# Kernel tuning notes

Measured on AMD Instinct MI355X. Metric: run time of the kernel, lower is better.

## Reference

```python
import jax, jax.numpy as jnp
import numpy as np

B, S, H = 16, 2048, 1024
N_EXAMPLES, MEM_LEN = 16, 128


def setup_inputs() -> dict:
    key = jax.random.key(0)
    k1, k2, k3, k4 = jax.random.split(key, 4)
    return {
        "seq_vectors": jax.random.normal(k1, (B, S, H), dtype=jnp.float32),
        "attention_mask": jax.random.randint(k2, (B, S), 0, 2, dtype=jnp.int32),
        "memory_vectors": jax.random.normal(k3, (B, N_EXAMPLES, MEM_LEN, H), dtype=jnp.float32),
        "memory_attention_mask": jax.random.randint(k4, (B, N_EXAMPLES, MEM_LEN), 0, 2, dtype=jnp.int32),
    }


def reference(seq_vectors, attention_mask, memory_vectors, memory_attention_mask):
    b, s, h = seq_vectors.shape
    # flatten memory: [B, N, H] with N = n_examples * mem_len
    mem = memory_vectors.reshape(b, -1, h)
    mmask = memory_attention_mask.reshape(b, -1)
    # zero out masked memory rows (mask-via-zero, not additive -inf)
    mem = jnp.where((mmask == 0)[:, :, None], jnp.zeros((), mem.dtype), mem)
    # FAITHFUL to original: view(batch, hidden, -1) is a RESHAPE of the
    # contiguous [B, N, H] buffer into [B, H, N], NOT a transpose.
    mem_reshaped = mem.reshape(b, h, -1)  # [B, H, N]
    scores = jnp.einsum("bsh,bhn->bsn", seq_vectors, mem_reshaped)  # [B, S, N]
    probs = jax.nn.softmax(scores, axis=-1)
    attention_vectors = jnp.einsum("bsn,bnh->bsh", probs, mem)
    return seq_vectors + attention_vectors
```

## Files before the change

kernel.cpp:

```cpp
#include <hip/hip_runtime.h>
#include <cstdint>
#include <cstddef>

#define Bn 16
#define Sn 2048
#define Hn 1024
#define Nn 2048

typedef unsigned short u16;
typedef float  f32x4  __attribute__((ext_vector_type(4)));
typedef int    i32x4  __attribute__((ext_vector_type(4)));
typedef short  s16x8  __attribute__((ext_vector_type(8)));
typedef unsigned char  u8x4  __attribute__((ext_vector_type(4)));
typedef unsigned char  u8x8  __attribute__((ext_vector_type(8)));

__device__ __forceinline__ void quant2(float x, char& q1, char& q2) {
  float f1 = rintf(x * 16.f);
  f1 = fminf(127.f, fmaxf(-127.f, f1));
  float r = x - f1 * 0.0625f;
  float f2 = rintf(r * 2048.f);
  f2 = fminf(127.f, fmaxf(-127.f, f2));
  q1 = (char)(int)f1;
  q2 = (char)(int)f2;
}

__device__ __forceinline__ char quant1(float x) {
  float f = rintf(x * 16.f);
  f = fminf(127.f, fmaxf(-127.f, f));
  return (char)(int)f;
}

__device__ __forceinline__ void stage64Bb(const char* gbase, int pitchBytes, void* ldsbase, int lane) {
  const int gsrc = (lane & 3) ^ ((lane >> 3) & 3);
  const char* gp = gbase + (size_t)(lane >> 2) * pitchBytes + gsrc * 16;
  __builtin_amdgcn_global_load_lds(
      (__attribute__((address_space(1))) void*)gp,
      (__attribute__((address_space(3))) void*)ldsbase, 16, 0, 0);
}


__global__ __launch_bounds__(256) void prep_seq_i8(const float* __restrict__ seq,
                                                   char* __restrict__ a1, char* __restrict__ a2) {
  size_t i = (size_t)blockIdx.x * 256 + threadIdx.x;
  float4 v = ((const float4*)seq)[i];
  float x[4] = {v.x, v.y, v.z, v.w};
  u8x4 p1, p2;
#pragma unroll
  for (int j = 0; j < 4; ++j) {
    char q1, q2;
    quant2(x[j], q1, q2);
    p1[j] = (unsigned char)q1;
    p2[j] = (unsigned char)q2;
  }
  ((u8x4*)a1)[i] = p1;
  ((u8x4*)a2)[i] = p2;
}

__global__ __launch_bounds__(256) void prep_bt(const float* __restrict__ mem,
                                               const int* __restrict__ mmask,
                                               char* __restrict__ b1o, char* __restrict__ b2o,
                                               char* __restrict__ memq) {
  __shared__ float tile[64][33];
  const int b = blockIdx.z;
  const int r0 = blockIdx.x * 64;
  const int c0 = blockIdx.y * 32;
  const int tx = threadIdx.x & 31, ty = threadIdx.x >> 5;
  const float* src = mem + (size_t)b * (Nn * Hn);
  const int* mk = mmask + b * Nn;
#pragma unroll
  for (int j = 0; j < 8; ++j) {
    int r = r0 + ty + j * 8;
    float v = src[(size_t)r * Hn + c0 + tx];
    v = mk[r] ? v : 0.f;
    tile[ty + j * 8][tx] = v;
  }
  __syncthreads();
  {
    const int nr = threadIdx.x >> 2;
    const int hb = (threadIdx.x & 3) * 8;
    u8x8 ov;
#pragma unroll
    for (int j = 0; j < 8; ++j) ov[j] = (unsigned char)quant1(tile[nr][hb + j]);
    *(u8x8*)(memq + (size_t)b * Nn * Hn + (size_t)(r0 + nr) * Hn + c0 + hb) = ov;
  }
  {
    const int cl = threadIdx.x & 31;
    const int p  = (threadIdx.x >> 5) & 1;
    const int q  = threadIdx.x >> 6;
    u8x8 o1, o2;
#pragma unroll
    for (int j = 0; j < 8; ++j) {
      char q1, q2;
      quant2(tile[2 * (q * 8 + j) + p][cl], q1, q2);
      o1[j] = (unsigned char)q1;
      o2[j] = (unsigned char)q2;
    }
    size_t o = (size_t)b * Nn * Hn + (size_t)(p * 1024 + c0 + cl) * Hn + (r0 >> 1) + q * 8;
    *(u8x8*)(b1o + o) = o1;
    *(u8x8*)(b2o + o) = o2;
  }
}

__global__ __launch_bounds__(256, 3) void gemm_scores_coarse(
    const char* __restrict__ A1, const char* __restrict__ B1,
    short* __restrict__ C) {
  __shared__ __align__(16) char ldsm[49152];
  const int b = blockIdx.z;
  const int lid = blockIdx.x + (blockIdx.y << 4);
  const int xcd = lid & 7, idx = lid >> 3;
  const int tn = ((xcd & 1) << 3) | (idx & 7);
  const int tm = ((xcd >> 1) << 2) | (idx >> 3);
  const int tid = threadIdx.x;
  const int w = tid >> 6, l = tid & 63;
  const int wr = w >> 1, wc = w & 1;
  const size_t aOff = (size_t)(b * Sn + tm * 128) * Hn;
  const size_t bOff = (size_t)(b * Nn + tn * 128) * Hn;

  i32x4 acc[4][4] = {};

  const int gRd = ((l >> 4) ^ ((l >> 1) & 3)) * 16;
  const int ao = (wr * 64 + (l & 15)) * 64 + gRd;
  const int bo = (wc * 64 + (l & 15)) * 64 + gRd;

  auto stageStep = [&](int kk, char* buf) {
    const int kb = kk * 64;
#pragma unroll
    for (int i = 0; i < 2; ++i) {
      const int rb = w * 32 + i * 16;
      const size_t ro = (size_t)rb * Hn + kb;
      stage64Bb(A1 + aOff + ro, Hn, buf + rb * 64, l);
      stage64Bb(B1 + bOff + ro, Hn, buf + 8192 + rb * 64, l);
    }
  };

  stageStep(0, ldsm);
  stageStep(1, ldsm + 16384);

  int cb = 0;
  for (int kk = 0; kk < 16; ++kk) {
    char* cur = ldsm + cb * 16384;
    int sb = cb + 2; if (sb >= 3) sb -= 3;
    if (kk <= 14) asm volatile("s_waitcnt vmcnt(4)" ::: "memory");
    else          asm volatile("s_waitcnt vmcnt(0)" ::: "memory");
    __builtin_amdgcn_s_barrier();
    asm volatile("" ::: "memory");
    __builtin_amdgcn_sched_barrier(0);
    i32x4 bfr[4];
#pragma unroll
    for (int ni = 0; ni < 4; ++ni) bfr[ni] = *(const i32x4*)(cur + 8192 + bo + ni * 1024);
    i32x4 afr[4];
#pragma unroll
    for (int mi = 0; mi < 4; ++mi) afr[mi] = *(const i32x4*)(cur + ao + mi * 1024);
    if (kk + 2 < 16) stageStep(kk + 2, ldsm + sb * 16384);
    __builtin_amdgcn_s_setprio(1);
#pragma unroll
    for (int mi = 0; mi < 4; ++mi)
#pragma unroll
      for (int ni = 0; ni < 4; ++ni)
        acc[mi][ni] = __builtin_amdgcn_mfma_i32_16x16x64_i8(afr[mi], bfr[ni], acc[mi][ni], 0, 0, 0);
    __builtin_amdgcn_s_setprio(0);
    cb = (cb + 1 == 3) ? 0 : cb + 1;
  }
  const int r0 = tm * 128 + wr * 64 + (l >> 4) * 4;
  const int c0 = tn * 128 + wc * 64 + (l & 15);
#pragma unroll
  for (int mi = 0; mi < 4; ++mi)
#pragma unroll
    for (int ni = 0; ni < 4; ++ni) {
      size_t base = (size_t)(b * Sn + r0 + mi * 16) * Nn + c0 + ni * 16;
#pragma unroll
      for (int j = 0; j < 4; ++j) {
        int s = (int)rintf((float)acc[mi][ni][j] * 0.5f);
        s = s > 32767 ? 32767 : (s < -32767 ? -32767 : s);
        C[base + (size_t)j * Nn] = (short)s;
      }
    }
}

__global__ __launch_bounds__(256) void softmax_attn(
    const short* __restrict__ sc,
    const char* __restrict__ memq,
    const char* __restrict__ B1q, const char* __restrict__ B2q,
    const char* __restrict__ A1q, const char* __restrict__ A2q,
    float* __restrict__ out) {
  __shared__ int redi[4];
  __shared__ int wtot[4];
  __shared__ unsigned short sidx[64];
  __shared__ int scand[64];
  __shared__ int scross[64];
  __shared__ unsigned char sp[64];
  const size_t row = blockIdx.x;
  const int b = (int)(row >> 11);
  const int t = threadIdx.x;
  const int w = t >> 6, l = t & 63;
  s16x8 v = ((const s16x8*)(sc + row * Nn))[t];
  int mymax = (int)v[0];
#pragma unroll
  for (int j = 1; j < 8; ++j) mymax = max(mymax, (int)v[j]);
  for (int o = 32; o > 0; o >>= 1) mymax = max(mymax, __shfl_xor(mymax, o));
  if (l == 0) redi[w] = mymax;
  __syncthreads();
  const int mc = max(max(redi[0], redi[1]), max(redi[2], redi[3]));
  const int thresh = mc - 1408;
  int cnt = 0;
#pragma unroll
  for (int j = 0; j < 8; ++j) cnt += ((int)v[j] >= thresh);
  int incl = cnt;
  for (int o = 1; o < 64; o <<= 1) {
    int xv = __shfl_up(incl, o);
    if (l >= o) incl += xv;
  }
  if (l == 63) wtot[w] = incl;
  __syncthreads();
  int base = 0;
#pragma unroll
  for (int wq = 0; wq < 4; ++wq) if (wq < w) base += wtot[wq];
  int pos = base + incl - cnt;
#pragma unroll
  for (int j = 0; j < 8; ++j)
    if ((int)v[j] >= thresh) {
      if (pos < 64) { sidx[pos] = (unsigned short)(t * 8 + j); scand[pos] = (int)v[j]; }
      pos++;
    }
  __syncthreads();
  int total = wtot[0] + wtot[1] + wtot[2] + wtot[3];
  if (total > 64) total = 64;
  const i32x4 a1s = *(const i32x4*)(A1q + row * (size_t)Hn + l * 16);
  const i32x4 a2s = *(const i32x4*)(A2q + row * (size_t)Hn + l * 16);
  for (int k0 = 0; k0 < total; k0 += 4) {
    const int k = k0 + w;
    int cross = 0;
    if (k < total) {
      const size_t nb = ((size_t)b * Nn + sidx[k]) * Hn + l * 16;
      const i32x4 b1v = *(const i32x4*)(B1q + nb);
      const i32x4 b2v = *(const i32x4*)(B2q + nb);
#pragma unroll
      for (int r = 0; r < 4; ++r)
#pragma unroll
        for (int s8 = 0; s8 < 4; ++s8) {
          const int sh = s8 * 8;
          cross += (int)(char)(a1s[r] >> sh) * (int)(char)(b2v[r] >> sh)
                 + (int)(char)(a2s[r] >> sh) * (int)(char)(b1v[r] >> sh);
        }
    }
    for (int o = 32; o > 0; o >>= 1) cross += __shfl_xor(cross, o);
    if (l == 0 && k < total) scross[k] = cross;
  }
  __syncthreads();
  if (t < total) {
    float mref = -1e30f;
    for (int k = 0; k < total; ++k) {
      float f = (float)scand[k] * 0.0078125f + (float)scross[k] * (1.f / 32768.f);
      mref = fmaxf(mref, f);
    }
    float s = 0.f;
    for (int k = 0; k < total; ++k) {
      float f = (float)scand[k] * 0.0078125f + (float)scross[k] * (1.f / 32768.f);
      s += __expf(f - mref);
    }
    const float fme = (float)scand[t] * 0.0078125f + (float)scross[t] * (1.f / 32768.f);
    sp[t] = (unsigned char)(int)rintf(127.f * __expf(fme - mref) / s);
  }
  __syncthreads();
  const char* mq = memq + (size_t)b * (Nn * Hn);
  int a0 = 0, a1v = 0, a2v = 0, a3 = 0;
  for (int k = 0; k < total; ++k) {
    const int pw = sp[k];
    if (!pw) continue;
    const int n = sidx[k];
    const int wv = *(const int*)(mq + (size_t)n * Hn + (t << 2));
    a0 += pw * (int)(char)(wv);
    a1v += pw * (int)(char)(wv >> 8);
    a2v += pw * (int)(char)(wv >> 16);
    a3 += pw * (int)(char)(wv >> 24);
  }
  const size_t obase = row * Hn + (size_t)(t << 2);
  const int w1 = *(const int*)(A1q + obase);
  const int w2 = *(const int*)(A2q + obase);
  const float scl = 1.f / 2032.f;
  float4 o;
  o.x = (float)(char)(w1)       * 0.0625f + (float)(char)(w2)       * (1.f / 2048.f) + (float)a0 * scl;
  o.y = (float)(char)(w1 >> 8)  * 0.0625f + (float)(char)(w2 >> 8)  * (1.f / 2048.f) + (float)a1v * scl;
  o.z = (float)(char)(w1 >> 16) * 0.0625f + (float)(char)(w2 >> 16) * (1.f / 2048.f) + (float)a2v * scl;
  o.w = (float)(char)(w1 >> 24) * 0.0625f + (float)(char)(w2 >> 24) * (1.f / 2048.f) + (float)a3 * scl;
  *(float4*)(out + obase) = o;
}

__global__ void ws_fail(float* out) {
  size_t i = (size_t)blockIdx.x * blockDim.x + threadIdx.x;
  size_t stride = (size_t)gridDim.x * blockDim.x;
  for (; i < (size_t)Bn * Sn * Hn; i += stride) out[i] = 12345.0f;
}

extern "C" void kernel_launch(void* const* d_in, const int* in_sizes, int n_in,
                              void* d_out, int out_size, void* d_ws, size_t ws_size,
                              hipStream_t stream) {
  const float* seq = (const float*)d_in[0];
  const float* mem = (const float*)d_in[2];
  const int* mmask = (const int*)d_in[3];
  float* out = (float*)d_out;

  const size_t MiB = 1024 * 1024;
  const size_t perB = 18 * MiB;
  int BC = 16;
  while (BC > 1 && (size_t)BC * perB > ws_size) BC >>= 1;
  if ((size_t)BC * perB > ws_size) {
    ws_fail<<<2048, 256, 0, stream>>>(out);
    return;
  }

  char* ws = (char*)d_ws;
  const size_t SEG8 = (size_t)BC * Sn * Hn;
  char* a1 = ws;
  char* a2 = ws + SEG8;
  char* b1 = ws + 2 * SEG8;
  char* b2 = ws + 3 * SEG8;
  char* memq = ws + 4 * SEG8;
  short* scores = (short*)(ws + 5 * SEG8);

  for (int b0 = 0; b0 < Bn; b0 += BC) {
    const float* seqb = seq + (size_t)b0 * Sn * Hn;
    const float* memb = mem + (size_t)b0 * Nn * Hn;
    const int* mkb = mmask + (size_t)b0 * Nn;
    float* outb = out + (size_t)b0 * Sn * Hn;

    prep_seq_i8<<<dim3(BC * Sn * Hn / 4 / 256), 256, 0, stream>>>(seqb, a1, a2);
    prep_bt<<<dim3(Nn / 64, Hn / 32, BC), 256, 0, stream>>>(memb, mkb, b1, b2, memq);
    gemm_scores_coarse<<<dim3(Nn / 128, Sn / 128, BC), 256, 0, stream>>>(a1, b1, scores);
    softmax_attn<<<dim3(BC * Sn), 256, 0, stream>>>(scores, memq, b1, b2, a1, a2, outb);
  }
}
```

Baseline: 362.8 us.

## Emit per-tile row maxima from scores GEMM to skip reading full score rows

The scores GEMM epilogue now reduces each row's maximum across its 128-column tile and writes it to a small per-row/per-tile buffer. The softmax kernel reads these 16 tile maxima to get the row max, then only loads the score tiles whose maximum reaches the threshold, instead of reading the whole 2048-wide score row. This is meant to cut score-buffer reads in the softmax stage. In exchange it adds shuffle and LDS reduction work to the GEMM epilogue and a serialized per-tile loop with three barriers per tile in softmax.

```diff
diff --git a/kernel.cpp b/kernel.cpp
--- a/kernel.cpp
+++ b/kernel.cpp
@@ -103,8 +103,9 @@
 
 __global__ __launch_bounds__(256, 3) void gemm_scores_coarse(
     const char* __restrict__ A1, const char* __restrict__ B1,
-    short* __restrict__ C) {
+    short* __restrict__ C, short* __restrict__ gtmax) {
   __shared__ __align__(16) char ldsm[49152];
+  __shared__ short tmx[2][128];
   const int b = blockIdx.z;
   const int lid = blockIdx.x + (blockIdx.y << 4);
   const int xcd = lid & 7, idx = lid >> 3;
@@ -175,16 +176,50 @@
         C[base + (size_t)j * Nn] = (short)s;
       }
     }
+  int rmax[4][4];
+#pragma unroll
+  for (int mi = 0; mi < 4; ++mi)
+#pragma unroll
+    for (int j = 0; j < 4; ++j) {
+      int mv = acc[mi][0][j];
+#pragma unroll
+      for (int ni = 1; ni < 4; ++ni) mv = max(mv, acc[mi][ni][j]);
+      rmax[mi][j] = mv;
+    }
+#pragma unroll
+  for (int o = 1; o < 16; o <<= 1)
+#pragma unroll
+    for (int mi = 0; mi < 4; ++mi)
+#pragma unroll
+      for (int j = 0; j < 4; ++j)
+        rmax[mi][j] = max(rmax[mi][j], __shfl_xor(rmax[mi][j], o));
+  if ((l & 15) == 0) {
+#pragma unroll
+    for (int mi = 0; mi < 4; ++mi)
+#pragma unroll
+      for (int j = 0; j < 4; ++j) {
+        int s = (int)rintf((float)rmax[mi][j] * 0.5f);
+        s = s > 32767 ? 32767 : (s < -32767 ? -32767 : s);
+        tmx[wc][wr * 64 + mi * 16 + (l >> 4) * 4 + j] = (short)s;
+      }
+  }
+  __syncthreads();
+  if (tid < 128) {
+    short mA = tmx[0][tid], mB = tmx[1][tid];
+    gtmax[(size_t)(b * Sn + tm * 128 + tid) * 16 + tn] = mA > mB ? mA : mB;
+  }
 }
 
 __global__ __launch_bounds__(256) void softmax_attn(
     const short* __restrict__ sc,
+    const short* __restrict__ tmax,
     const char* __restrict__ memq,
     const char* __restrict__ B1q, const char* __restrict__ B2q,
     const char* __restrict__ A1q, const char* __restrict__ A2q,
     float* __restrict__ out) {
-  __shared__ int redi[4];
+  __shared__ short sh16[16];
   __shared__ int wtot[4];
+  __shared__ int ncand_s;
   __shared__ unsigned short sidx[64];
   __shared__ int scand[64];
   __shared__ int scross[64];
@@ -193,38 +228,41 @@
   const int b = (int)(row >> 11);
   const int t = threadIdx.x;
   const int w = t >> 6, l = t & 63;
-  s16x8 v = ((const s16x8*)(sc + row * Nn))[t];
-  int mymax = (int)v[0];
-#pragma unroll
-  for (int j = 1; j < 8; ++j) mymax = max(mymax, (int)v[j]);
-  for (int o = 32; o > 0; o >>= 1) mymax = max(mymax, __shfl_xor(mymax, o));
-  if (l == 0) redi[w] = mymax;
-  __syncthreads();
-  const int mc = max(max(redi[0], redi[1]), max(redi[2], redi[3]));
+  if (t < 16) sh16[t] = tmax[row * 16 + t];
+  if (t == 0) ncand_s = 0;
+  __syncthreads();
+  int mc = -32768;
+#pragma unroll
+  for (int i = 0; i < 16; ++i) mc = max(mc, (int)sh16[i]);
   const int thresh = mc - 1408;
-  int cnt = 0;
-#pragma unroll
-  for (int j = 0; j < 8; ++j) cnt += ((int)v[j] >= thresh);
-  int incl = cnt;
-  for (int o = 1; o < 64; o <<= 1) {
-    int xv = __shfl_up(incl, o);
-    if (l >= o) incl += xv;
-  }
-  if (l == 63) wtot[w] = incl;
-  __syncthreads();
-  int base = 0;
-#pragma unroll
-  for (int wq = 0; wq < 4; ++wq) if (wq < w) base += wtot[wq];
-  int pos = base + incl - cnt;
-#pragma unroll
-  for (int j = 0; j < 8; ++j)
-    if ((int)v[j] >= thresh) {
-      if (pos < 64) { sidx[pos] = (unsigned short)(t * 8 + j); scand[pos] = (int)v[j]; }
-      pos++;
-    }
-  __syncthreads();
-  int total = wtot[0] + wtot[1] + wtot[2] + wtot[3];
-  if (total > 64) total = 64;
+  for (int ti = 0; ti < 16; ++ti) {
+    if ((int)sh16[ti] < thresh) continue;
+    int sval = 0, flag = 0;
+    if (t < 128) {
+      sval = (int)sc[row * (size_t)Nn + ti * 128 + t];
+      flag = (sval >= thresh) ? 1 : 0;
+    }
+    int incl = flag;
+    for (int o = 1; o < 64; o <<= 1) {
+      int xv = __shfl_up(incl, o);
+      if (l >= o) incl += xv;
+    }
+    if (l == 63) wtot[w] = incl;
+    __syncthreads();
+    const int base2 = ncand_s;
+    int basew = 0;
+#pragma unroll
+    for (int wq = 0; wq < 4; ++wq) if (wq < w) basew += wtot[wq];
+    const int pos = base2 + basew + incl - flag;
+    if (flag && pos < 64) { sidx[pos] = (unsigned short)(ti * 128 + t); scand[pos] = sval; }
+    __syncthreads();
+    if (t == 0) {
+      int nn = base2 + wtot[0] + wtot[1] + wtot[2] + wtot[3];
+      ncand_s = nn > 64 ? 64 : nn;
+    }
+    __syncthreads();
+  }
+  const int total = ncand_s;
   const i32x4 a1s = *(const i32x4*)(A1q + row * (size_t)Hn + l * 16);
   const i32x4 a2s = *(const i32x4*)(A2q + row * (size_t)Hn + l * 16);
   for (int k0 = 0; k0 < total; k0 += 4) {
@@ -301,7 +339,7 @@
   float* out = (float*)d_out;
 
   const size_t MiB = 1024 * 1024;
-  const size_t perB = 18 * MiB;
+  const size_t perB = 18 * MiB + 64 * 1024;
   int BC = 16;
   while (BC > 1 && (size_t)BC * perB > ws_size) BC >>= 1;
   if ((size_t)BC * perB > ws_size) {
@@ -317,6 +355,7 @@
   char* b2 = ws + 3 * SEG8;
   char* memq = ws + 4 * SEG8;
   short* scores = (short*)(ws + 5 * SEG8);
+  short* tmaxb = (short*)(ws + 9 * SEG8);
 
   for (int b0 = 0; b0 < Bn; b0 += BC) {
     const float* seqb = seq + (size_t)b0 * Sn * Hn;
@@ -326,7 +365,7 @@
 
     prep_seq_i8<<<dim3(BC * Sn * Hn / 4 / 256), 256, 0, stream>>>(seqb, a1, a2);
     prep_bt<<<dim3(Nn / 64, Hn / 32, BC), 256, 0, stream>>>(memb, mkb, b1, b2, memq);
-    gemm_scores_coarse<<<dim3(Nn / 128, Sn / 128, BC), 256, 0, stream>>>(a1, b1, scores);
-    softmax_attn<<<dim3(BC * Sn), 256, 0, stream>>>(scores, memq, b1, b2, a1, a2, outb);
-  }
-}
+    gemm_scores_coarse<<<dim3(Nn / 128, Sn / 128, BC), 256, 0, stream>>>(a1, b1, scores, tmaxb);
+    softmax_attn<<<dim3(BC * Sn), 256, 0, stream>>>(scores, tmaxb, memq, b1, b2, a1, a2, outb);
+  }
+}
```

New measurement: 425.7 us. 17.3% more time.
